# Performance work log

Hardware: AMD Instinct MI355X
Metric: run time of the kernel (lower is better)

## Reference

```python
import jax, jax.numpy as jnp
import numpy as np

C = 512
NUM_HEADS = 8
GROUPS = 32
EPS = 1e-5


def setup_inputs() -> dict:
    key = jax.random.key(0)
    ks = jax.random.split(key, 7)
    B, H, W = 8, 32, 32
    x = jax.random.normal(ks[0], (B, C, H, W), dtype=jnp.float32)
    gn_w = jnp.ones((C,), dtype=jnp.float32)
    gn_b = jnp.zeros((C,), dtype=jnp.float32)
    # 1x1 convs as dense matrices [out, in]
    qkv_w = jax.random.normal(ks[1], (3 * C, C), dtype=jnp.float32) * (1.0 / np.sqrt(C))
    qkv_b = jnp.zeros((3 * C,), dtype=jnp.float32)
    proj_w = jax.random.normal(ks[2], (C, C), dtype=jnp.float32) * (1.0 / np.sqrt(C))
    proj_b = jnp.zeros((C,), dtype=jnp.float32)
    return {"x": x, "gn_w": gn_w, "gn_b": gn_b, "qkv_w": qkv_w,
            "qkv_b": qkv_b, "proj_w": proj_w, "proj_b": proj_b}


def reference(x, gn_w, gn_b, qkv_w, qkv_b, proj_w, proj_b):
    B, Cc, H, W = x.shape
    nh = NUM_HEADS
    d = Cc // nh
    N = H * W

    # GroupNorm(32, C) with affine
    xg = x.reshape(B, GROUPS, Cc // GROUPS, H, W)
    mean = jnp.mean(xg, axis=(2, 3, 4), keepdims=True)
    var = jnp.var(xg, axis=(2, 3, 4), keepdims=True)
    hn = ((xg - mean) * jax.lax.rsqrt(var + EPS)).reshape(B, Cc, H, W)
    hn = hn * gn_w[None, :, None, None] + gn_b[None, :, None, None]

    # 1x1 conv QKV projection: [B, 3C, H, W]
    qkv = jnp.einsum('oc,bchw->bohw', qkv_w, hn) + qkv_b[None, :, None, None]
    q, k, v = jnp.split(qkv, 3, axis=1)

    def to_heads(t):  # [B, C, H, W] -> [B, nh, N, d]
        return t.reshape(B, nh, d, N).transpose(0, 1, 3, 2)

    q, k, v = to_heads(q), to_heads(k), to_heads(v)
    scale = d ** (-0.5)
    attn = jax.nn.softmax(jnp.einsum('bhnd,bhmd->bhnm', q, k) * scale, axis=-1)
    o = jnp.einsum('bhnm,bhmd->bhnd', attn, v)          # [B, nh, N, d]
    o = o.transpose(0, 1, 3, 2).reshape(B, Cc, H, W)

    # 1x1 conv output projection + residual
    o = jnp.einsum('oc,bchw->bohw', proj_w, o) + proj_b[None, :, None, None]
    return x + o
```

## Files before the change

kernel.cpp:

```cpp
#include <hip/hip_runtime.h>

typedef __bf16 bf16x8 __attribute__((ext_vector_type(8)));
typedef float f32x4 __attribute__((ext_vector_type(4)));

#define MFMA(a, b, c) __builtin_amdgcn_mfma_f32_16x16x32_bf16(a, b, c, 0, 0, 0)

#define CS 0.18033688011112042f

__device__ __forceinline__ ushort f2bf(float f) {
    __bf16 h = (__bf16)f;
    return *(ushort*)&h;
}

__device__ __forceinline__ void stage_tile64(ushort* lds, const ushort* gbase,
                                             int row_stride, int nchunks,
                                             int wave, int lane) {
    int r8 = lane >> 3;
    int cswz = ((lane & 7) ^ r8) << 4;
#pragma unroll
    for (int c = wave; c < nchunks; c += 4) {
        const char* g = (const char*)(gbase + (size_t)(c * 8 + r8) * row_stride) + cswz;
        __builtin_amdgcn_global_load_lds(
            (const __attribute__((address_space(1))) unsigned int*)g,
            (__attribute__((address_space(3))) unsigned int*)((char*)lds + c * 1024),
            16, 0, 0);
    }
}

__device__ __forceinline__ bf16x8 lds_read_row(const ushort* lds, int row, int cb) {
    return *(const bf16x8*)((const char*)lds + row * 128 + (cb ^ ((row & 7) << 4)));
}

__device__ __forceinline__ void stage_tile32(ushort* lds, const ushort* gbase,
                                             int row_stride, int nchunks,
                                             int wave, int lane) {
    int r16 = lane >> 2;
    int csw = (((lane & 3) ^ ((lane >> 3) & 3)) << 3);
#pragma unroll
    for (int c = wave; c < nchunks; c += 4) {
        const ushort* g = gbase + (size_t)(c * 16 + r16) * row_stride + csw;
        __builtin_amdgcn_global_load_lds(
            (const __attribute__((address_space(1))) unsigned int*)g,
            (__attribute__((address_space(3))) unsigned int*)((char*)lds + c * 1024),
            16, 0, 0);
    }
}

__device__ __forceinline__ bf16x8 lds_read_row32(const ushort* lds, int row, int cb) {
    return *(const bf16x8*)((const char*)lds + row * 64 + (cb ^ (((row >> 1) & 3) << 4)));
}

__global__ __launch_bounds__(256) void gn_cvt_kernel(const float* __restrict__ x,
                                                     const float* __restrict__ gnw,
                                                     const float* __restrict__ gnb,
                                                     ushort* __restrict__ hnT,
                                                     const float* __restrict__ w1,
                                                     const float* __restrict__ w2,
                                                     ushort* __restrict__ o1,
                                                     ushort* __restrict__ o2) {
    if (blockIdx.x >= 256) {
        int t = (blockIdx.x - 256) * 256 + threadIdx.x;
        const int n1q = (1536 * 512) / 4;
        float4 v;
        ushort* dst;
        int idx;
        if (t < n1q) {
            v = ((const float4*)w1)[t]; dst = o1; idx = t;
        } else {
            idx = t - n1q;
            v = ((const float4*)w2)[idx]; dst = o2;
        }
        ushort4 p;
        p.x = f2bf(v.x); p.y = f2bf(v.y); p.z = f2bf(v.z); p.w = f2bf(v.w);
        ((ushort4*)dst)[idx] = p;
        return;
    }

    int b = blockIdx.x >> 5, g = blockIdx.x & 31;
    const float* xp = x + (size_t)(b * 512 + g * 16) * 1024;
    int t = threadIdx.x;

    float s = 0.f, ss = 0.f;
    const float4* xp4 = (const float4*)xp;
    for (int i = t; i < 4096; i += 256) {
        float4 v = xp4[i];
        s += (v.x + v.y) + (v.z + v.w);
        ss += (v.x * v.x + v.y * v.y) + (v.z * v.z + v.w * v.w);
    }
#pragma unroll
    for (int off = 32; off >= 1; off >>= 1) {
        s += __shfl_xor(s, off);
        ss += __shfl_xor(ss, off);
    }
    __shared__ float red[8];
    __shared__ float sw[16], sb[16];
    int wave = t >> 6;
    if ((t & 63) == 0) { red[wave] = s; red[wave + 4] = ss; }
    if (t < 16) { sw[t] = gnw[g * 16 + t]; sb[t] = gnb[g * 16 + t]; }
    __syncthreads();
    float S = red[0] + red[1] + red[2] + red[3];
    float SS = red[4] + red[5] + red[6] + red[7];
    float mean = S * (1.0f / 16384.0f);
    float var = SS * (1.0f / 16384.0f) - mean * mean;
    float rstd = rsqrtf(var + 1e-5f);

    __shared__ ushort tile[16][258];
    int cc0 = (t & 3) * 4;
    int nb = t >> 2;
    for (int chunk = 0; chunk < 4; ++chunk) {
        __syncthreads();
#pragma unroll
        for (int cc = 0; cc < 16; ++cc) {
            float v = xp[cc * 1024 + chunk * 256 + t];
            tile[cc][t] = f2bf((v - mean) * rstd * sw[cc] + sb[cc]);
        }
        __syncthreads();
        size_t rowbase = (size_t)b * 1024 + chunk * 256;
#pragma unroll
        for (int k = 0; k < 4; ++k) {
            int nl = nb + 64 * k;
            ushort4 p;
            p.x = tile[cc0 + 0][nl];
            p.y = tile[cc0 + 1][nl];
            p.z = tile[cc0 + 2][nl];
            p.w = tile[cc0 + 3][nl];
            *(ushort4*)(hnT + (rowbase + nl) * 512 + g * 16 + cc0) = p;
        }
    }
}

__global__ __launch_bounds__(256) void gemm_qkv(const ushort* __restrict__ Wb,
                                                const ushort* __restrict__ hnT,
                                                const float* __restrict__ qkvb,
                                                ushort* __restrict__ qT,
                                                ushort* __restrict__ kT,
                                                ushort* __restrict__ vb) {
    int lane = threadIdx.x & 63, wave = threadIdx.x >> 6;
    int l15 = lane & 15, lg = lane >> 4;
    int bi = blockIdx.x;
    int b = bi & 7;
    int slot = bi >> 3;
    int m0 = (slot % 12) * 128;
    int n0 = (slot / 12) * 128;
    int mw = (wave >> 1) * 64, nw = (wave & 1) * 64;
    const ushort* Ag = Wb + (size_t)m0 * 512;
    const ushort* Bg = hnT + (size_t)b * 524288 + (size_t)n0 * 512;

    __shared__ ushort abuf[4][4096];
    __shared__ ushort bbuf[4][4096];

    f32x4 acc[4][4] = {};
#pragma unroll
    for (int p = 0; p < 3; ++p) {
        stage_tile32(abuf[p], Ag + p * 32, 512, 8, wave, lane);
        stage_tile32(bbuf[p], Bg + p * 32, 512, 8, wave, lane);
    }
    asm volatile("s_waitcnt vmcnt(8)" ::: "memory");
    __builtin_amdgcn_s_barrier();

#pragma unroll 1
    for (int t = 0; t < 16; ++t) {
        if (t < 13) {
            int nxt = (t + 3) & 3;
            stage_tile32(abuf[nxt], Ag + (t + 3) * 32, 512, 8, wave, lane);
            stage_tile32(bbuf[nxt], Bg + (t + 3) * 32, 512, 8, wave, lane);
        }
        const ushort* A = abuf[t & 3];
        const ushort* B = bbuf[t & 3];
        bf16x8 af[4], bfr[4];
#pragma unroll
        for (int i = 0; i < 4; i++)
            af[i] = lds_read_row32(A, mw + i * 16 + l15, lg * 16);
#pragma unroll
        for (int j = 0; j < 4; j++)
            bfr[j] = lds_read_row32(B, nw + j * 16 + l15, lg * 16);
        __builtin_amdgcn_s_setprio(1);
#pragma unroll
        for (int i = 0; i < 4; i++)
#pragma unroll
            for (int j = 0; j < 4; j++)
                acc[i][j] = MFMA(af[i], bfr[j], acc[i][j]);
        __builtin_amdgcn_s_setprio(0);
        if (t < 15) {
            if (t < 13)      asm volatile("s_waitcnt vmcnt(8)" ::: "memory");
            else if (t == 13) asm volatile("s_waitcnt vmcnt(4)" ::: "memory");
            else              asm volatile("s_waitcnt vmcnt(0)" ::: "memory");
            __builtin_amdgcn_s_barrier();
        }
    }

#pragma unroll
    for (int i = 0; i < 4; i++) {
        int ob = m0 + mw + i * 16 + lg * 4;
        float bias[4];
#pragma unroll
        for (int r = 0; r < 4; r++) bias[r] = qkvb[ob + r];
        int part = ob >> 9;
        int oo = ob & 511;
#pragma unroll
        for (int j = 0; j < 4; j++) {
            int n = n0 + nw + j * 16 + l15;
            if (part == 2) {
                int L = n & 63;
                int cf = L >> 4;
                int s = ((cf >> 1) << 5) | (((L >> 2) & 3) << 3) | ((cf & 1) << 2) | (L & 3);
                int np = (n & ~63) | s;
#pragma unroll
                for (int r = 0; r < 4; r++)
                    vb[(size_t)(b * 512 + oo + r) * 1024 + np] = f2bf(acc[i][j][r] + bias[r]);
            } else {
                ushort* dst = part ? kT : qT;
                float sc = part ? 1.0f : CS;
                int h = oo >> 6, dd = oo & 63;
                ushort4 p;
                p.x = f2bf((acc[i][j][0] + bias[0]) * sc);
                p.y = f2bf((acc[i][j][1] + bias[1]) * sc);
                p.z = f2bf((acc[i][j][2] + bias[2]) * sc);
                p.w = f2bf((acc[i][j][3] + bias[3]) * sc);
                *(ushort4*)(dst + ((size_t)((b * 8 + h) * 1024 + n)) * 64 + dd) = p;
            }
        }
    }
}

__global__ __launch_bounds__(256) void attn_kernel(const ushort* __restrict__ qT,
                                                   const ushort* __restrict__ kT,
                                                   const ushort* __restrict__ vb,
                                                   ushort* __restrict__ aoT) {
    int bi = blockIdx.x;
    int bh = ((bi >> 6) << 3) | (bi & 7);
    int q0 = ((bi >> 3) & 7) * 128;
    int b = bh >> 3, h = bh & 7;
    int lane = threadIdx.x & 63, wave = threadIdx.x >> 6;
    int l15 = lane & 15, lg = lane >> 4;
    const ushort* qp = qT + (size_t)bh * 65536;
    const ushort* kp = kT + (size_t)bh * 65536;
    const ushort* vp = vb + (size_t)bh * 65536;

    __shared__ ushort kbuf[3][4096];
    __shared__ ushort vbuf[3][4096];

    bf16x8 vone;
#pragma unroll
    for (int e = 0; e < 8; e++) vone[e] = (__bf16)1.0f;

    bf16x8 qf[2][2];
#pragma unroll
    for (int i = 0; i < 2; i++)
#pragma unroll
        for (int kh = 0; kh < 2; kh++)
            qf[i][kh] = *(const bf16x8*)(qp + (size_t)(q0 + wave * 32 + i * 16 + l15) * 64 + kh * 32 + lg * 8);

    f32x4 oacc[2][4] = {};
    f32x4 lacc[2] = {};

    stage_tile64(kbuf[0], kp, 64, 8, wave, lane);
    stage_tile64(vbuf[0], vp, 1024, 8, wave, lane);
    stage_tile64(kbuf[1], kp + 4096, 64, 8, wave, lane);
    stage_tile64(vbuf[1], vp + 64, 1024, 8, wave, lane);
    asm volatile("s_waitcnt vmcnt(4)" ::: "memory");
    __builtin_amdgcn_s_barrier();

    int cur = 0;
#pragma unroll 1
    for (int t = 0; t < 16; ++t) {
        if (t < 14) {
            int nxt = cur + 2; if (nxt >= 3) nxt -= 3;
            stage_tile64(kbuf[nxt], kp + (size_t)(t + 2) * 4096, 64, 8, wave, lane);
            stage_tile64(vbuf[nxt], vp + (t + 2) * 64, 1024, 8, wave, lane);
        }
        const ushort* kb = kbuf[cur];
        const ushort* vc = vbuf[cur];

        f32x4 sacc[2][4] = {};
        __builtin_amdgcn_s_setprio(1);
#pragma unroll
        for (int kh = 0; kh < 2; kh++)
#pragma unroll
            for (int cf = 0; cf < 4; cf++) {
                bf16x8 kf = lds_read_row(kb, cf * 16 + l15, kh * 64 + lg * 16);
                sacc[0][cf] = MFMA(kf, qf[0][kh], sacc[0][cf]);
                sacc[1][cf] = MFMA(kf, qf[1][kh], sacc[1][cf]);
            }
        __builtin_amdgcn_s_setprio(0);

        bf16x8 vf[2][4];
#pragma unroll
        for (int ks = 0; ks < 2; ks++)
#pragma unroll
            for (int cf = 0; cf < 4; cf++)
                vf[ks][cf] = lds_read_row(vc, cf * 16 + l15, ks * 64 + lg * 16);

        bf16x8 pa[2][2];
#pragma unroll
        for (int i = 0; i < 2; i++)
#pragma unroll
            for (int ks = 0; ks < 2; ks++) {
                bf16x8 tr;
#pragma unroll
                for (int jhi = 0; jhi < 2; jhi++)
#pragma unroll
                    for (int r = 0; r < 4; r++)
                        tr[jhi * 4 + r] = (__bf16)exp2f(sacc[i][ks * 2 + jhi][r]);
                pa[i][ks] = tr;
            }

        __builtin_amdgcn_s_setprio(1);
#pragma unroll
        for (int i = 0; i < 2; i++)
#pragma unroll
            for (int ks = 0; ks < 2; ks++) {
                lacc[i] = MFMA(pa[i][ks], vone, lacc[i]);
#pragma unroll
                for (int cf = 0; cf < 4; cf++)
                    oacc[i][cf] = MFMA(pa[i][ks], vf[ks][cf], oacc[i][cf]);
            }
        __builtin_amdgcn_s_setprio(0);

        if (t < 15) {
            if (t < 14) asm volatile("s_waitcnt vmcnt(4)" ::: "memory");
            else        asm volatile("s_waitcnt vmcnt(0)" ::: "memory");
            __builtin_amdgcn_s_barrier();
        }
        cur = cur + 1; if (cur == 3) cur = 0;
    }

#pragma unroll
    for (int i = 0; i < 2; i++)
#pragma unroll
        for (int r = 0; r < 4; r++) {
            float inv = 1.0f / lacc[i][r];
            int n = q0 + wave * 32 + i * 16 + lg * 4 + r;
            size_t obase = ((size_t)b * 1024 + n) * 512 + h * 64;
#pragma unroll
            for (int cf = 0; cf < 4; cf++)
                aoT[obase + cf * 16 + l15] = f2bf(oacc[i][cf][r] * inv);
        }
}

__global__ __launch_bounds__(256) void gemm_proj(const ushort* __restrict__ Wb,
                                                 const ushort* __restrict__ aoT,
                                                 const float* __restrict__ projb,
                                                 const float* __restrict__ x,
                                                 float* __restrict__ out) {
    int lane = threadIdx.x & 63, wave = threadIdx.x >> 6;
    int l15 = lane & 15, lg = lane >> 4;
    int bi = blockIdx.x;
    int b = bi & 7;
    int slot = bi >> 3;
    int m0 = (slot & 3) * 128;
    int n0 = (slot >> 2) * 64;
    int mw = (wave >> 1) * 64, nw = (wave & 1) * 32;
    const ushort* Ag = Wb + (size_t)m0 * 512;
    const ushort* Bg = aoT + (size_t)b * 524288 + (size_t)n0 * 512;

    __shared__ ushort abuf[4][4096];
    __shared__ ushort bbuf[4][2048];

    f32x4 acc[4][2] = {};
#pragma unroll
    for (int p = 0; p < 3; ++p) {
        stage_tile32(abuf[p], Ag + p * 32, 512, 8, wave, lane);
        stage_tile32(bbuf[p], Bg + p * 32, 512, 4, wave, lane);
    }
    asm volatile("s_waitcnt vmcnt(6)" ::: "memory");
    __builtin_amdgcn_s_barrier();

#pragma unroll 1
    for (int t = 0; t < 16; ++t) {
        if (t < 13) {
            int nxt = (t + 3) & 3;
            stage_tile32(abuf[nxt], Ag + (t + 3) * 32, 512, 8, wave, lane);
            stage_tile32(bbuf[nxt], Bg + (t + 3) * 32, 512, 4, wave, lane);
        }
        const ushort* A = abuf[t & 3];
        const ushort* B = bbuf[t & 3];
        bf16x8 af[4], bfr[2];
#pragma unroll
        for (int i = 0; i < 4; i++)
            af[i] = lds_read_row32(A, mw + i * 16 + l15, lg * 16);
#pragma unroll
        for (int j = 0; j < 2; j++)
            bfr[j] = lds_read_row32(B, nw + j * 16 + l15, lg * 16);
        __builtin_amdgcn_s_setprio(1);
#pragma unroll
        for (int i = 0; i < 4; i++)
#pragma unroll
            for (int j = 0; j < 2; j++)
                acc[i][j] = MFMA(af[i], bfr[j], acc[i][j]);
        __builtin_amdgcn_s_setprio(0);
        if (t < 15) {
            if (t < 13)      asm volatile("s_waitcnt vmcnt(6)" ::: "memory");
            else if (t == 13) asm volatile("s_waitcnt vmcnt(3)" ::: "memory");
            else              asm volatile("s_waitcnt vmcnt(0)" ::: "memory");
            __builtin_amdgcn_s_barrier();
        }
    }

#pragma unroll
    for (int i = 0; i < 4; i++) {
        int ob = m0 + mw + i * 16 + lg * 4;
        float bias[4];
#pragma unroll
        for (int r = 0; r < 4; r++) bias[r] = projb[ob + r];
#pragma unroll
        for (int j = 0; j < 2; j++) {
            int n = n0 + nw + j * 16 + l15;
#pragma unroll
            for (int r = 0; r < 4; r++) {
                size_t idx = (size_t)(b * 512 + ob + r) * 1024 + n;
                out[idx] = x[idx] + bias[r] + acc[i][j][r];
            }
        }
    }
}

extern "C" void kernel_launch(void* const* d_in, const int* in_sizes, int n_in,
                              void* d_out, int out_size, void* d_ws, size_t ws_size,
                              hipStream_t stream) {
    const float* x     = (const float*)d_in[0];
    const float* gnw   = (const float*)d_in[1];
    const float* gnb   = (const float*)d_in[2];
    const float* qkvw  = (const float*)d_in[3];
    const float* qkvb  = (const float*)d_in[4];
    const float* projw = (const float*)d_in[5];
    const float* projb = (const float*)d_in[6];
    float* out = (float*)d_out;

    char* ws = (char*)d_ws;
    ushort* hnT    = (ushort*)(ws);
    ushort* qT     = (ushort*)(ws + (size_t)(8u << 20));
    ushort* kT     = (ushort*)(ws + (size_t)(16u << 20));
    ushort* vbuf   = (ushort*)(ws + (size_t)(24u << 20));
    ushort* qkvwb  = (ushort*)(ws + (size_t)(32u << 20));
    ushort* projwb = (ushort*)(ws + (size_t)(32u << 20) + 1572864);

    gn_cvt_kernel<<<dim3(1280), dim3(256), 0, stream>>>(x, gnw, gnb, hnT,
                                                        qkvw, projw, qkvwb, projwb);
    gemm_qkv<<<dim3(768), dim3(256), 0, stream>>>(qkvwb, hnT, qkvb, qT, kT, vbuf);
    attn_kernel<<<dim3(512), dim3(256), 0, stream>>>(qT, kT, vbuf, hnT );
    gemm_proj<<<dim3(512), dim3(256), 0, stream>>>(projwb, hnT, projb, x, out);
}
```

Baseline: 86.38 us.

## Cache GroupNorm input in LDS as bf16 and cut QKV GEMM pipeline to 3 stages

The GroupNorm kernel now stores x as bf16 in shared memory during the statistics pass, then normalizes from LDS with folded scale and bias. This avoids reading x from global memory a second time and drops the per-chunk barriers. The QKV GEMM goes from a 4-buffer to a 3-buffer LDS pipeline and adds a 3-blocks-per-SM launch bound, trading prefetch depth for occupancy. Rounding x to bf16 before normalization adds a small extra precision loss.

```diff
diff --git a/kernel.cpp b/kernel.cpp
--- a/kernel.cpp
+++ b/kernel.cpp
@@ -10,6 +10,10 @@
 __device__ __forceinline__ ushort f2bf(float f) {
     __bf16 h = (__bf16)f;
     return *(ushort*)&h;
+}
+__device__ __forceinline__ float bf2f(ushort u) {
+    unsigned int x = ((unsigned int)u) << 16;
+    return __uint_as_float(x);
 }
 
 __device__ __forceinline__ void stage_tile64(ushort* lds, const ushort* gbase,
@@ -58,6 +62,10 @@
                                                      const float* __restrict__ w2,
                                                      ushort* __restrict__ o1,
                                                      ushort* __restrict__ o2) {
+    __shared__ ushort xcache[16 * 1028];
+    __shared__ float red[8];
+    __shared__ float sw[16], sb[16];
+
     if (blockIdx.x >= 256) {
         int t = (blockIdx.x - 256) * 256 + threadIdx.x;
         const int n1q = (1536 * 512) / 4;
@@ -86,14 +94,17 @@
         float4 v = xp4[i];
         s += (v.x + v.y) + (v.z + v.w);
         ss += (v.x * v.x + v.y * v.y) + (v.z * v.z + v.w * v.w);
+        int f = i * 4;
+        int cc = f >> 10, nl = f & 1023;
+        ushort4 c;
+        c.x = f2bf(v.x); c.y = f2bf(v.y); c.z = f2bf(v.z); c.w = f2bf(v.w);
+        *(ushort4*)&xcache[cc * 1028 + nl] = c;
     }
 #pragma unroll
     for (int off = 32; off >= 1; off >>= 1) {
         s += __shfl_xor(s, off);
         ss += __shfl_xor(ss, off);
     }
-    __shared__ float red[8];
-    __shared__ float sw[16], sb[16];
     int wave = t >> 6;
     if ((t & 63) == 0) { red[wave] = s; red[wave + 4] = ss; }
     if (t < 16) { sw[t] = gnw[g * 16 + t]; sb[t] = gnb[g * 16 + t]; }
@@ -104,37 +115,30 @@
     float var = SS * (1.0f / 16384.0f) - mean * mean;
     float rstd = rsqrtf(var + 1e-5f);
 
-    __shared__ ushort tile[16][258];
     int cc0 = (t & 3) * 4;
     int nb = t >> 2;
-    for (int chunk = 0; chunk < 4; ++chunk) {
-        __syncthreads();
-#pragma unroll
-        for (int cc = 0; cc < 16; ++cc) {
-            float v = xp[cc * 1024 + chunk * 256 + t];
-            tile[cc][t] = f2bf((v - mean) * rstd * sw[cc] + sb[cc]);
-        }
-        __syncthreads();
-        size_t rowbase = (size_t)b * 1024 + chunk * 256;
-#pragma unroll
-        for (int k = 0; k < 4; ++k) {
-            int nl = nb + 64 * k;
-            ushort4 p;
-            p.x = tile[cc0 + 0][nl];
-            p.y = tile[cc0 + 1][nl];
-            p.z = tile[cc0 + 2][nl];
-            p.w = tile[cc0 + 3][nl];
-            *(ushort4*)(hnT + (rowbase + nl) * 512 + g * 16 + cc0) = p;
-        }
-    }
-}
-
-__global__ __launch_bounds__(256) void gemm_qkv(const ushort* __restrict__ Wb,
-                                                const ushort* __restrict__ hnT,
-                                                const float* __restrict__ qkvb,
-                                                ushort* __restrict__ qT,
-                                                ushort* __restrict__ kT,
-                                                ushort* __restrict__ vb) {
+    float w0 = sw[cc0] * rstd, w1_ = sw[cc0 + 1] * rstd,
+          w2_ = sw[cc0 + 2] * rstd, w3 = sw[cc0 + 3] * rstd;
+    float b0 = sb[cc0] - mean * w0, b1 = sb[cc0 + 1] - mean * w1_,
+          b2 = sb[cc0 + 2] - mean * w2_, b3 = sb[cc0 + 3] - mean * w3;
+#pragma unroll
+    for (int k = 0; k < 16; ++k) {
+        int nl = nb + 64 * k;
+        ushort4 p;
+        p.x = f2bf(bf2f(xcache[(cc0 + 0) * 1028 + nl]) * w0 + b0);
+        p.y = f2bf(bf2f(xcache[(cc0 + 1) * 1028 + nl]) * w1_ + b1);
+        p.z = f2bf(bf2f(xcache[(cc0 + 2) * 1028 + nl]) * w2_ + b2);
+        p.w = f2bf(bf2f(xcache[(cc0 + 3) * 1028 + nl]) * w3 + b3);
+        *(ushort4*)(hnT + ((size_t)b * 1024 + nl) * 512 + g * 16 + cc0) = p;
+    }
+}
+
+__global__ __launch_bounds__(256, 3) void gemm_qkv(const ushort* __restrict__ Wb,
+                                                   const ushort* __restrict__ hnT,
+                                                   const float* __restrict__ qkvb,
+                                                   ushort* __restrict__ qT,
+                                                   ushort* __restrict__ kT,
+                                                   ushort* __restrict__ vb) {
     int lane = threadIdx.x & 63, wave = threadIdx.x >> 6;
     int l15 = lane & 15, lg = lane >> 4;
     int bi = blockIdx.x;
@@ -146,27 +150,28 @@
     const ushort* Ag = Wb + (size_t)m0 * 512;
     const ushort* Bg = hnT + (size_t)b * 524288 + (size_t)n0 * 512;
 
-    __shared__ ushort abuf[4][4096];
-    __shared__ ushort bbuf[4][4096];
+    __shared__ ushort abuf[3][4096];
+    __shared__ ushort bbuf[3][4096];
 
     f32x4 acc[4][4] = {};
 #pragma unroll
-    for (int p = 0; p < 3; ++p) {
+    for (int p = 0; p < 2; ++p) {
         stage_tile32(abuf[p], Ag + p * 32, 512, 8, wave, lane);
         stage_tile32(bbuf[p], Bg + p * 32, 512, 8, wave, lane);
     }
-    asm volatile("s_waitcnt vmcnt(8)" ::: "memory");
+    asm volatile("s_waitcnt vmcnt(4)" ::: "memory");
     __builtin_amdgcn_s_barrier();
 
+    int cur = 0;
 #pragma unroll 1
     for (int t = 0; t < 16; ++t) {
-        if (t < 13) {
-            int nxt = (t + 3) & 3;
-            stage_tile32(abuf[nxt], Ag + (t + 3) * 32, 512, 8, wave, lane);
-            stage_tile32(bbuf[nxt], Bg + (t + 3) * 32, 512, 8, wave, lane);
-        }
-        const ushort* A = abuf[t & 3];
-        const ushort* B = bbuf[t & 3];
+        if (t < 14) {
+            int nxt = cur + 2; if (nxt >= 3) nxt -= 3;
+            stage_tile32(abuf[nxt], Ag + (t + 2) * 32, 512, 8, wave, lane);
+            stage_tile32(bbuf[nxt], Bg + (t + 2) * 32, 512, 8, wave, lane);
+        }
+        const ushort* A = abuf[cur];
+        const ushort* B = bbuf[cur];
         bf16x8 af[4], bfr[4];
 #pragma unroll
         for (int i = 0; i < 4; i++)
@@ -182,11 +187,11 @@
                 acc[i][j] = MFMA(af[i], bfr[j], acc[i][j]);
         __builtin_amdgcn_s_setprio(0);
         if (t < 15) {
-            if (t < 13)      asm volatile("s_waitcnt vmcnt(8)" ::: "memory");
-            else if (t == 13) asm volatile("s_waitcnt vmcnt(4)" ::: "memory");
-            else              asm volatile("s_waitcnt vmcnt(0)" ::: "memory");
+            if (t < 14) asm volatile("s_waitcnt vmcnt(4)" ::: "memory");
+            else        asm volatile("s_waitcnt vmcnt(0)" ::: "memory");
             __builtin_amdgcn_s_barrier();
         }
+        cur = cur + 1; if (cur == 3) cur = 0;
     }
 
 #pragma unroll
```

After: 80.20 us. 7.2% less time.
